# Optimization experiments

Measured on AMD Instinct MI355X. Metric: run time of the kernel, lower is better.

Reference implementation:

```python
import jax, jax.numpy as jnp
import numpy as np

N_NODES = 50000
N_EDGES = 800000
IN_DIM = 64
HID = 128
NUM_GRAPHS = 256


def setup_inputs() -> dict:
    key = jax.random.key(0)
    ks = jax.random.split(key, 20)
    inp = {
        'x': jax.random.normal(ks[0], (N_NODES, IN_DIM), dtype=jnp.float32),
        'edge_index': jax.random.randint(ks[1], (2, N_EDGES), 0, N_NODES, dtype=jnp.int32),
        'batch_idx': jnp.sort(jax.random.randint(ks[2], (N_NODES,), 0, NUM_GRAPHS, dtype=jnp.int32)),
    }
    # GIN layer MLP params (3 layers): Linear(in,hid)->ReLU->Linear(hid,hid)
    dims = [(IN_DIM, HID), (HID, HID), (HID, HID)]
    ki = 3
    for li, (di, dh) in enumerate(dims):
        s1 = 1.0 / np.sqrt(di)
        s2 = 1.0 / np.sqrt(dh)
        inp[f'gin{li}_w1'] = jax.random.uniform(ks[ki], (di, dh), jnp.float32, -s1, s1); ki += 1
        inp[f'gin{li}_b1'] = jnp.zeros((dh,), jnp.float32)
        inp[f'gin{li}_w2'] = jax.random.uniform(ks[ki], (dh, dh), jnp.float32, -s2, s2); ki += 1
        inp[f'gin{li}_b2'] = jnp.zeros((dh,), jnp.float32)
    # head: Linear(2*HID, HID) -> ReLU -> (Dropout eval=id) -> Linear(HID, 1)
    sh = 1.0 / np.sqrt(2 * HID)
    so = 1.0 / np.sqrt(HID)
    inp['head_w1'] = jax.random.uniform(ks[ki], (2 * HID, HID), jnp.float32, -sh, sh); ki += 1
    inp['head_b1'] = jnp.zeros((HID,), jnp.float32)
    inp['head_w2'] = jax.random.uniform(ks[ki], (HID, 1), jnp.float32, -so, so); ki += 1
    inp['head_b2'] = jnp.zeros((1,), jnp.float32)
    return inp


def _gin_layer(h, src, dst, w1, b1, w2, b2):
    # GINConv with eps=0: mlp(x + sum_{j->i} x_j), followed by outer ReLU
    agg = jax.ops.segment_sum(h[src], dst, num_segments=N_NODES)
    z = h + agg
    z = jnp.dot(jax.nn.relu(jnp.dot(z, w1) + b1), w2) + b2
    return jax.nn.relu(z)


def reference(x, edge_index, batch_idx,
              gin0_w1, gin0_b1, gin0_w2, gin0_b2,
              gin1_w1, gin1_b1, gin1_w2, gin1_b2,
              gin2_w1, gin2_b1, gin2_w2, gin2_b2,
              head_w1, head_b1, head_w2, head_b2):
    src, dst = edge_index[0], edge_index[1]
    h = _gin_layer(x, src, dst, gin0_w1, gin0_b1, gin0_w2, gin0_b2)
    h = _gin_layer(h, src, dst, gin1_w1, gin1_b1, gin1_w2, gin1_b2)
    h = _gin_layer(h, src, dst, gin2_w1, gin2_b1, gin2_w2, gin2_b2)
    # meanmax readout over graphs
    cnt = jax.ops.segment_sum(jnp.ones((h.shape[0],), h.dtype), batch_idx,
                              num_segments=NUM_GRAPHS)  # [G]
    ssum = jax.ops.segment_sum(h, batch_idx, num_segments=NUM_GRAPHS)  # [G, HID]
    mean_pool = ssum / jnp.maximum(cnt, 1.0)[:, None]
    max_pool = jax.ops.segment_max(h, batch_idx, num_segments=NUM_GRAPHS)
    max_pool = jnp.where(cnt[:, None] > 0, max_pool, 0.0)
    graph_repr = jnp.concatenate([mean_pool, max_pool], axis=-1)  # [G, 2*HID]
    # fraud head (dropout is identity in eval)
    hh = jax.nn.relu(jnp.dot(graph_repr, head_w1) + head_b1)
    logits = jnp.dot(hh, head_w2) + head_b2  # [G, 1]
    score = jax.nn.sigmoid(logits)
    return score
```

## Files before the change

### kernel.cpp

```cpp
#include <hip/hip_runtime.h>
#include <hip/hip_bf16.h>

#define N_NODES   50000
#define N_EDGES   800000
#define IN_DIM    64
#define HID       128
#define NUM_GRAPHS 256
#define NBUCK     196
#define BCAP      8192
#define CPAD      16

typedef __bf16 bf16x8 __attribute__((ext_vector_type(8)));
typedef unsigned short u16x8 __attribute__((ext_vector_type(8)));
typedef float f32x4 __attribute__((ext_vector_type(4)));

__device__ __forceinline__ float b2f(unsigned short u) {
    return __uint_as_float(((unsigned int)u) << 16);
}
__device__ __forceinline__ unsigned short f2b(float f) {
    unsigned int x = __float_as_uint(f);
    x = (x + 0x7fffu + ((x >> 16) & 1u)) >> 16;
    return (unsigned short)x;
}

__global__ void diag_kernel(unsigned short* out, unsigned short pat) {
    out[threadIdx.x] = pat;
}

__global__ __launch_bounds__(256) void mega_pre_kernel(
    const unsigned short* __restrict__ x,
    const void* w0, const void* w1, const void* w2,
    const void* w3, const void* w4, const void* w5,
    unsigned short* __restrict__ wfbase,
    const int* __restrict__ batch, int* __restrict__ gstart,
    float* __restrict__ psum, unsigned int* __restrict__ pmax,
    const void* hw1, unsigned short* __restrict__ w1t,
    int* __restrict__ bcursor, int* __restrict__ flagp) {
    int b = blockIdx.x;
    int tid = threadIdx.x;

    if (b < 352) {
        __shared__ int cnt;
        if (tid == 0) cnt = 0;
        __syncthreads();
        unsigned short u = x[2 * tid];
        int e = (u >> 7) & 0xff;
        if (e <= 100 || e >= 140) atomicAdd(&cnt, 1);
        __syncthreads();
        int flag = cnt > 64;

        int mat, boff;
        if (b < 32) { mat = 0; boff = b; }
        else { mat = 1 + (b - 32) / 64; boff = (b - 32) % 64; }
        const void* W = mat == 0 ? w0 : mat == 1 ? w1 : mat == 2 ? w2
                      : mat == 3 ? w3 : mat == 4 ? w4 : w5;
        int KC = (mat == 0) ? 2 : 4;
        int idx = boff * 256 + tid;
        int j  = idx & 7;
        int l  = (idx >> 3) & 63;
        int tc = idx >> 9;
        int c  = tc % KC;
        int t  = tc / KC;
        int k  = c * 32 + (l >> 4) * 8 + j;
        int n  = t * 16 + (l & 15);
        unsigned short v = flag ? f2b(((const float*)W)[k * 128 + n])
                                : ((const unsigned short*)W)[k * 128 + n];
        wfbase[mat * 16384 + idx] = v;
    } else if (b < 548) {
        int i = (b - 352) * 256 + tid;
        if (i < NUM_GRAPHS * HID) { psum[i] = 0.0f; pmax[i] = 0u; }
        if (i >= N_NODES) return;
        int b1 = batch[i];
        int b0 = (i == 0) ? -1 : batch[i - 1];
        for (int g = b0 + 1; g <= b1; g++) gstart[g] = i;
        if (i == N_NODES - 1)
            for (int g = b1 + 1; g <= NUM_GRAPHS; g++) gstart[g] = N_NODES;
    } else if (b < 580) {
        __shared__ int cnt;
        if (tid == 0) cnt = 0;
        __syncthreads();
        unsigned short u = x[2 * tid];
        int e = (u >> 7) & 0xff;
        if (e <= 100 || e >= 140) atomicAdd(&cnt, 1);
        __syncthreads();
        int flag = cnt > 64;
        int base = (b - 548) * 1024;
#pragma unroll
        for (int j = 0; j < 4; j++) {
            int idx = base + j * 256 + tid;
            int n = idx >> 8;
            int k = idx & 255;
            unsigned short v = flag ? f2b(((const float*)hw1)[k * 128 + n])
                                    : ((const unsigned short*)hw1)[k * 128 + n];
            w1t[idx] = v;
        }
    } else {
        if (tid < NBUCK) bcursor[tid * CPAD] = tid * BCAP;
        __shared__ int cnt;
        if (tid == 0) cnt = 0;
        __syncthreads();
        int c = 0;
        for (int j = 0; j < 16; j++) {
            unsigned short u = x[2 * (tid * 16 + j)];
            int e = (u >> 7) & 0xff;
            if (e <= 100 || e >= 140) c++;
        }
        atomicAdd(&cnt, c);
        __syncthreads();
        if (tid == 0) *flagp = (cnt > 1024) ? 1 : 0;
    }
}

__global__ __launch_bounds__(1024) void bscatter_kernel(const int* __restrict__ src,
        const int* __restrict__ dst, int* __restrict__ bcursor,
        unsigned int* __restrict__ ebuf) {
    __shared__ int lcnt[NBUCK];
    __shared__ int lbase[NBUCK];
    __shared__ int lcur[NBUCK];
    int tid = threadIdx.x;
    if (tid < NBUCK) lcnt[tid] = 0;
    __syncthreads();
    int e0 = blockIdx.x * 4096;
    int d[4], s[4];
#pragma unroll
    for (int k = 0; k < 4; k++) {
        int e = e0 + k * 1024 + tid;
        if (e < N_EDGES) {
            d[k] = dst[e]; s[k] = src[e];
            atomicAdd(&lcnt[d[k] >> 8], 1);
        } else d[k] = -1;
    }
    __syncthreads();
    if (tid < NBUCK) {
        int c = lcnt[tid];
        lbase[tid] = c ? atomicAdd(&bcursor[tid * CPAD], c) : 0;
        lcur[tid] = 0;
    }
    __syncthreads();
#pragma unroll
    for (int k = 0; k < 4; k++) {
        if (d[k] >= 0) {
            int b = d[k] >> 8;
            int p = lbase[b] + atomicAdd(&lcur[b], 1);
            ebuf[p] = ((unsigned int)(d[k] & 255) << 16) | (unsigned int)s[k];
        }
    }
}

__global__ __launch_bounds__(512) void bsort_kernel(const unsigned int* __restrict__ ebuf,
        const int* __restrict__ bcursor, int* __restrict__ off,
        unsigned short* __restrict__ csr) {
    __shared__ int cntA[256];
    __shared__ int sc[256];
    __shared__ int lcnt[256];
    __shared__ int lcur[256];
    int b = blockIdx.x, tid = threadIdx.x;

    if (tid < 256) {
        int v = (tid < NBUCK) ? (bcursor[tid * CPAD] - tid * BCAP) : 0;
        cntA[tid] = v;
        sc[tid] = v;
    }
    __syncthreads();
    for (int d = 1; d < 256; d <<= 1) {
        int t = (tid >= d && tid < 256) ? sc[tid - d] : 0;
        __syncthreads();
        if (tid < 256) sc[tid] += t;
        __syncthreads();
    }
    int base = sc[b] - cntA[b];
    int cnt  = cntA[b];
    int ebase = b * BCAP;
    __syncthreads();

    if (tid < 256) lcnt[tid] = 0;
    __syncthreads();
    for (int i = tid; i < cnt; i += 512)
        atomicAdd(&lcnt[ebuf[ebase + i] >> 16], 1);
    __syncthreads();
    int v2 = 0;
    if (tid < 256) {
        v2 = lcnt[tid];
        sc[tid] = v2;
    }
    __syncthreads();
    for (int d = 1; d < 256; d <<= 1) {
        int t = (tid >= d && tid < 256) ? sc[tid - d] : 0;
        __syncthreads();
        if (tid < 256) sc[tid] += t;
        __syncthreads();
    }
    if (tid < 256) {
        int excl = sc[tid] - v2;
        lcur[tid] = excl;
        int node = b * 256 + tid;
        if (node < N_NODES) off[node] = base + excl;
    }
    if (b == 0 && tid == 0) off[N_NODES] = N_EDGES;
    __syncthreads();
    for (int i = tid; i < cnt; i += 512) {
        unsigned int ev = ebuf[ebase + i];
        int p = atomicAdd(&lcur[ev >> 16], 1);
        csr[base + p] = (unsigned short)(ev & 0xffffu);
    }
}

template <int K1, bool POOL, bool FROMX>
__global__ __launch_bounds__(256, 3) void fused_gin_kernel(
    const void* __restrict__ X,
    const int* __restrict__ off, const unsigned short* __restrict__ csr,
    const unsigned short* __restrict__ Wf1, const void* __restrict__ bias1,
    const unsigned short* __restrict__ Wf2, const void* __restrict__ bias2,
    unsigned short* __restrict__ Out, int M, const int* __restrict__ flagp,
    const int* __restrict__ batch, float* __restrict__ psum,
    unsigned int* __restrict__ pmax) {
    constexpr int KC1 = K1 / 32;
    __shared__ __align__(16) unsigned short lds_hi[64 * 136];
    __shared__ __align__(16) unsigned short lds_lo[64 * 136];
    __shared__ int batch_lds[64];

    int flag = *flagp;
    int wave = threadIdx.x >> 6;
    int lane = threadIdx.x & 63;
    int m_ = lane & 15;
    int q  = lane >> 4;

    if constexpr (POOL) {
        if (threadIdx.x < 64) {
            int gr = blockIdx.x * 64 + threadIdx.x;
            batch_lds[threadIdx.x] = gr < M ? batch[gr] : -1;
        }
    }

    int np = lane >> 4;
    int l  = lane & 15;
#pragma unroll 1
    for (int p = 0; p < 4; p++) {
        int nl = wave * 16 + p * 4 + np;
        int node = blockIdx.x * 64 + nl;
        int nodec = node < M ? node : (M - 1);
        int s = off[nodec], e = off[nodec + 1];
        if constexpr (FROMX) {
            float a0, a1, a2, a3;
            float b0 = 0.f, b1 = 0.f, b2 = 0.f, b3 = 0.f;
            float c0 = 0.f, c1 = 0.f, c2 = 0.f, c3 = 0.f;
            float d0 = 0.f, d1 = 0.f, d2 = 0.f, d3 = 0.f;
            if (flag) {
                const float4* xp = (const float4*)X;
                float4 u = xp[(size_t)nodec * 16 + l];
                a0 = u.x; a1 = u.y; a2 = u.z; a3 = u.w;
                int i = s;
                for (; i + 7 < e; i += 8) {
                    float4 v0 = xp[(size_t)csr[i] * 16 + l];
                    float4 v1 = xp[(size_t)csr[i + 1] * 16 + l];
                    float4 v2 = xp[(size_t)csr[i + 2] * 16 + l];
                    float4 v3 = xp[(size_t)csr[i + 3] * 16 + l];
                    float4 v4 = xp[(size_t)csr[i + 4] * 16 + l];
                    float4 v5 = xp[(size_t)csr[i + 5] * 16 + l];
                    float4 v6 = xp[(size_t)csr[i + 6] * 16 + l];
                    float4 v7 = xp[(size_t)csr[i + 7] * 16 + l];
                    a0 += v0.x; a1 += v0.y; a2 += v0.z; a3 += v0.w;
                    b0 += v1.x; b1 += v1.y; b2 += v1.z; b3 += v1.w;
                    c0 += v2.x; c1 += v2.y; c2 += v2.z; c3 += v2.w;
                    d0 += v3.x; d1 += v3.y; d2 += v3.z; d3 += v3.w;
                    a0 += v4.x; a1 += v4.y; a2 += v4.z; a3 += v4.w;
                    b0 += v5.x; b1 += v5.y; b2 += v5.z; b3 += v5.w;
                    c0 += v6.x; c1 += v6.y; c2 += v6.z; c3 += v6.w;
                    d0 += v7.x; d1 += v7.y; d2 += v7.z; d3 += v7.w;
                }
                for (; i + 3 < e; i += 4) {
                    float4 v0 = xp[(size_t)csr[i] * 16 + l];
                    float4 v1 = xp[(size_t)csr[i + 1] * 16 + l];
                    float4 v2 = xp[(size_t)csr[i + 2] * 16 + l];
                    float4 v3 = xp[(size_t)csr[i + 3] * 16 + l];
                    a0 += v0.x; a1 += v0.y; a2 += v0.z; a3 += v0.w;
                    b0 += v1.x; b1 += v1.y; b2 += v1.z; b3 += v1.w;
                    c0 += v2.x; c1 += v2.y; c2 += v2.z; c3 += v2.w;
                    d0 += v3.x; d1 += v3.y; d2 += v3.z; d3 += v3.w;
                }
                for (; i < e; i++) {
                    float4 v = xp[(size_t)csr[i] * 16 + l];
                    a0 += v.x; a1 += v.y; a2 += v.z; a3 += v.w;
                }
            } else {
                const ushort4* xp = (const ushort4*)X;
                ushort4 u = xp[(size_t)nodec * 16 + l];
                a0 = b2f(u.x); a1 = b2f(u.y); a2 = b2f(u.z); a3 = b2f(u.w);
                int i = s;
                for (; i + 7 < e; i += 8) {
                    ushort4 v0 = xp[(size_t)csr[i] * 16 + l];
                    ushort4 v1 = xp[(size_t)csr[i + 1] * 16 + l];
                    ushort4 v2 = xp[(size_t)csr[i + 2] * 16 + l];
                    ushort4 v3 = xp[(size_t)csr[i + 3] * 16 + l];
                    ushort4 v4 = xp[(size_t)csr[i + 4] * 16 + l];
                    ushort4 v5 = xp[(size_t)csr[i + 5] * 16 + l];
                    ushort4 v6 = xp[(size_t)csr[i + 6] * 16 + l];
                    ushort4 v7 = xp[(size_t)csr[i + 7] * 16 + l];
                    a0 += b2f(v0.x); a1 += b2f(v0.y); a2 += b2f(v0.z); a3 += b2f(v0.w);
                    b0 += b2f(v1.x); b1 += b2f(v1.y); b2 += b2f(v1.z); b3 += b2f(v1.w);
                    c0 += b2f(v2.x); c1 += b2f(v2.y); c2 += b2f(v2.z); c3 += b2f(v2.w);
                    d0 += b2f(v3.x); d1 += b2f(v3.y); d2 += b2f(v3.z); d3 += b2f(v3.w);
                    a0 += b2f(v4.x); a1 += b2f(v4.y); a2 += b2f(v4.z); a3 += b2f(v4.w);
                    b0 += b2f(v5.x); b1 += b2f(v5.y); b2 += b2f(v5.z); b3 += b2f(v5.w);
                    c0 += b2f(v6.x); c1 += b2f(v6.y); c2 += b2f(v6.z); c3 += b2f(v6.w);
                    d0 += b2f(v7.x); d1 += b2f(v7.y); d2 += b2f(v7.z); d3 += b2f(v7.w);
                }
                for (; i + 3 < e; i += 4) {
                    ushort4 v0 = xp[(size_t)csr[i] * 16 + l];
                    ushort4 v1 = xp[(size_t)csr[i + 1] * 16 + l];
                    ushort4 v2 = xp[(size_t)csr[i + 2] * 16 + l];
                    ushort4 v3 = xp[(size_t)csr[i + 3] * 16 + l];
                    a0 += b2f(v0.x); a1 += b2f(v0.y); a2 += b2f(v0.z); a3 += b2f(v0.w);
                    b0 += b2f(v1.x); b1 += b2f(v1.y); b2 += b2f(v1.z); b3 += b2f(v1.w);
                    c0 += b2f(v2.x); c1 += b2f(v2.y); c2 += b2f(v2.z); c3 += b2f(v2.w);
                    d0 += b2f(v3.x); d1 += b2f(v3.y); d2 += b2f(v3.z); d3 += b2f(v3.w);
                }
                for (; i < e; i++) {
                    ushort4 v = xp[(size_t)csr[i] * 16 + l];
                    a0 += b2f(v.x); a1 += b2f(v.y); a2 += b2f(v.z); a3 += b2f(v.w);
                }
            }
            ushort4 o;
            o.x = f2b(a0 + b0 + c0 + d0);
            o.y = f2b(a1 + b1 + c1 + d1);
            o.z = f2b(a2 + b2 + c2 + d2);
            o.w = f2b(a3 + b3 + c3 + d3);
            *reinterpret_cast<ushort4*>(&lds_hi[nl * 136 + l * 4]) = o;
        } else {
            const u16x8* hp = (const u16x8*)X;
            u16x8 u = hp[(size_t)nodec * 16 + l];
            float a[8], b[8], c[8], d[8];
#pragma unroll
            for (int j = 0; j < 8; j++) { a[j] = b2f(u[j]); b[j] = 0.f; c[j] = 0.f; d[j] = 0.f; }
            int i = s;
            for (; i + 7 < e; i += 8) {
                u16x8 v0 = hp[(size_t)csr[i] * 16 + l];
                u16x8 v1 = hp[(size_t)csr[i + 1] * 16 + l];
                u16x8 v2 = hp[(size_t)csr[i + 2] * 16 + l];
                u16x8 v3 = hp[(size_t)csr[i + 3] * 16 + l];
                u16x8 v4 = hp[(size_t)csr[i + 4] * 16 + l];
                u16x8 v5 = hp[(size_t)csr[i + 5] * 16 + l];
                u16x8 v6 = hp[(size_t)csr[i + 6] * 16 + l];
                u16x8 v7 = hp[(size_t)csr[i + 7] * 16 + l];
#pragma unroll
                for (int j = 0; j < 8; j++) {
                    a[j] += b2f(v0[j]); b[j] += b2f(v1[j]);
                    c[j] += b2f(v2[j]); d[j] += b2f(v3[j]);
                }
#pragma unroll
                for (int j = 0; j < 8; j++) {
                    a[j] += b2f(v4[j]); b[j] += b2f(v5[j]);
                    c[j] += b2f(v6[j]); d[j] += b2f(v7[j]);
                }
            }
            for (; i + 3 < e; i += 4) {
                u16x8 v0 = hp[(size_t)csr[i] * 16 + l];
                u16x8 v1 = hp[(size_t)csr[i + 1] * 16 + l];
                u16x8 v2 = hp[(size_t)csr[i + 2] * 16 + l];
                u16x8 v3 = hp[(size_t)csr[i + 3] * 16 + l];
#pragma unroll
                for (int j = 0; j < 8; j++) {
                    a[j] += b2f(v0[j]); b[j] += b2f(v1[j]);
                    c[j] += b2f(v2[j]); d[j] += b2f(v3[j]);
                }
            }
            for (; i < e; i++) {
                u16x8 v = hp[(size_t)csr[i] * 16 + l];
#pragma unroll
                for (int j = 0; j < 8; j++) a[j] += b2f(v[j]);
            }
            u16x8 o;
#pragma unroll
            for (int j = 0; j < 8; j++) o[j] = f2b(a[j] + b[j] + c[j] + d[j]);
            *reinterpret_cast<u16x8*>(&lds_hi[nl * 136 + l * 8]) = o;
        }
    }

    const unsigned short* wfl1 = Wf1 + lane * 8;
    const unsigned short* wfl2 = Wf2 + lane * 8;
    const unsigned short* zlds = &lds_hi[(wave * 16 + m_) * 136 + q * 8];

    bf16x8 afrag[KC1];
#pragma unroll
    for (int c = 0; c < KC1; c++)
        afrag[c] = *reinterpret_cast<const bf16x8*>(zlds + c * 32);

    float b1v[8], b2v[8];
#pragma unroll
    for (int t = 0; t < 8; t++) {
        int col = t * 16 + m_;
        b1v[t] = flag ? ((const float*)bias1)[col]
                      : b2f(((const unsigned short*)bias1)[col]);
        b2v[t] = flag ? ((const float*)bias2)[col]
                      : b2f(((const unsigned short*)bias2)[col]);
    }

    f32x4 acc[8];
#pragma unroll
    for (int t = 0; t < 8; t++) acc[t] = (f32x4)(0.0f);

    {
        bf16x8 wb[8], wn[8];
#pragma unroll
        for (int t = 0; t < 8; t++)
            wb[t] = *reinterpret_cast<const bf16x8*>(wfl1 + ((t * KC1 + 0) << 9));
#pragma unroll
        for (int c = 0; c < KC1; c++) {
            if (c + 1 < KC1) {
#pragma unroll
                for (int t = 0; t < 8; t++)
                    wn[t] = *reinterpret_cast<const bf16x8*>(wfl1 + ((t * KC1 + c + 1) << 9));
            }
#pragma unroll
            for (int t = 0; t < 8; t++)
                acc[t] = __builtin_amdgcn_mfma_f32_16x16x32_bf16(afrag[c], wb[t], acc[t], 0, 0, 0);
            if (c + 1 < KC1) {
#pragma unroll
                for (int t = 0; t < 8; t++) wb[t] = wn[t];
            }
        }
    }

#pragma unroll
    for (int r = 0; r < 4; r++) {
        int lr = wave * 16 + q * 4 + r;
#pragma unroll
        for (int t = 0; t < 8; t++) {
            int col = t * 16 + m_;
            float v = acc[t][r] + b1v[t];
            v = v > 0.0f ? v : 0.0f;
            unsigned short hb = f2b(v);
            lds_hi[lr * 136 + col] = hb;
            lds_lo[lr * 136 + col] = f2b(v - b2f(hb));
        }
    }

#pragma unroll
    for (int t = 0; t < 8; t++) acc[t] = (f32x4)(0.0f);

    {
        int lr2 = wave * 16 + m_;
        const unsigned short* hibase = &lds_hi[lr2 * 136 + q * 8];
        const unsigned short* lobase = &lds_lo[lr2 * 136 + q * 8];
        bf16x8 wb[8], wn[8];
#pragma unroll
        for (int t = 0; t < 8; t++)
            wb[t] = *reinterpret_cast<const bf16x8*>(wfl2 + ((t * 4 + 0) << 9));
#pragma unroll
        for (int c = 0; c < 4; c++) {
            if (c < 3) {
#pragma unroll
                for (int t = 0; t < 8; t++)
                    wn[t] = *reinterpret_cast<const bf16x8*>(wfl2 + ((t * 4 + c + 1) << 9));
            }
            bf16x8 ahi = *reinterpret_cast<const bf16x8*>(hibase + c * 32);
            bf16x8 alo = *reinterpret_cast<const bf16x8*>(lobase + c * 32);
#pragma unroll
            for (int t = 0; t < 8; t++) {
                acc[t] = __builtin_amdgcn_mfma_f32_16x16x32_bf16(ahi, wb[t], acc[t], 0, 0, 0);
                acc[t] = __builtin_amdgcn_mfma_f32_16x16x32_bf16(alo, wb[t], acc[t], 0, 0, 0);
            }
            if (c < 3) {
#pragma unroll
                for (int t = 0; t < 8; t++) wb[t] = wn[t];
            }
        }
    }

#pragma unroll
    for (int r = 0; r < 4; r++) {
        int lr = wave * 16 + q * 4 + r;
        int orow = blockIdx.x * 64 + lr;
#pragma unroll
        for (int t = 0; t < 8; t++) {
            int col = t * 16 + m_;
            float v = acc[t][r] + b2v[t];
            v = v > 0.0f ? v : 0.0f;
            if constexpr (POOL) {
                lds_hi[lr * 136 + col] = f2b(v);
            } else {
                if (orow < M) Out[(size_t)orow * HID + col] = f2b(v);
            }
        }
    }

    if constexpr (POOL) {
        __syncthreads();
        int f = threadIdx.x;
        if (f < HID) {
            int cur = -1;
            float sum = 0.0f, mx = 0.0f;
            for (int rrow = 0; rrow < 64; rrow++) {
                int g = batch_lds[rrow];
                if (g < 0) break;
                float v = b2f(lds_hi[rrow * 136 + f]);
                if (g == cur) {
                    sum += v;
                    mx = fmaxf(mx, v);
                } else {
                    if (cur >= 0) {
                        atomicAdd(&psum[cur * HID + f], sum);
                        atomicMax(&pmax[cur * HID + f], __float_as_uint(mx));
                    }
                    cur = g; sum = v; mx = v;
                }
            }
            if (cur >= 0) {
                atomicAdd(&psum[cur * HID + f], sum);
                atomicMax(&pmax[cur * HID + f], __float_as_uint(mx));
            }
        }
    }
}

__global__ __launch_bounds__(128) void head_kernel(
    const float* __restrict__ psum, const unsigned int* __restrict__ pmax,
    const int* __restrict__ gstart,
    const unsigned short* __restrict__ w1t,
    const void* __restrict__ b1, const void* __restrict__ w2,
    const void* __restrict__ b2,
    void* __restrict__ out, const int* __restrict__ flagp) {
    int g = blockIdx.x;
    int n = threadIdx.x;
    int flag = *flagp;
    __shared__ float repr[2 * HID];
    __shared__ float red[HID];

    float c = (float)(gstart[g + 1] - gstart[g]);
    float inv = 1.0f / fmaxf(c, 1.0f);
    repr[n]       = psum[g * HID + n] * inv;
    repr[HID + n] = __uint_as_float(pmax[g * HID + n]);
    __syncthreads();

    const u16x8* wp = (const u16x8*)(w1t + n * 256);
    float a0 = 0.f, a1 = 0.f, a2 = 0.f, a3 = 0.f;
#pragma unroll
    for (int c8 = 0; c8 < 32; c8 += 4) {
        u16x8 w0 = wp[c8 + 0];
        u16x8 w1 = wp[c8 + 1];
        u16x8 w2v = wp[c8 + 2];
        u16x8 w3 = wp[c8 + 3];
#pragma unroll
        for (int j = 0; j < 8; j++) {
            a0 += repr[(c8 + 0) * 8 + j] * b2f(w0[j]);
            a1 += repr[(c8 + 1) * 8 + j] * b2f(w1[j]);
            a2 += repr[(c8 + 2) * 8 + j] * b2f(w2v[j]);
            a3 += repr[(c8 + 3) * 8 + j] * b2f(w3[j]);
        }
    }
    float b1v = flag ? ((const float*)b1)[n] : b2f(((const unsigned short*)b1)[n]);
    float acc = a0 + a1 + a2 + a3 + b1v;
    acc = fmaxf(acc, 0.0f);

    float w2s = flag ? ((const float*)w2)[n] : b2f(((const unsigned short*)w2)[n]);
    red[n] = acc * w2s;
    __syncthreads();
    for (int s = 64; s > 0; s >>= 1) {
        if (n < s) red[n] += red[n + s];
        __syncthreads();
    }
    if (n == 0) {
        float b2v = flag ? ((const float*)b2)[0] : b2f(((const unsigned short*)b2)[0]);
        float logit = red[0] + b2v;
        float sv = 1.0f / (1.0f + expf(-logit));
        if (flag) ((float*)out)[g] = sv;
        else      ((unsigned short*)out)[g] = f2b(sv);
    }
}

extern "C" void kernel_launch(void* const* d_in, const int* in_sizes, int n_in,
                              void* d_out, int out_size, void* d_ws, size_t ws_size,
                              hipStream_t stream) {
    const int* edge = (const int*)d_in[1];
    const int* srcv = edge;
    const int* dstv = edge + N_EDGES;
    const int* batch = (const int*)d_in[2];

    char* ws = (char*)d_ws;
    unsigned short* A = (unsigned short*)ws;
    unsigned short* B = (unsigned short*)(ws + 12800000);
    unsigned int* ebuf = (unsigned int*)(ws + 25600000);
    unsigned short* csr = (unsigned short*)(ws + 32100000);
    int* off    = (int*)(ws + 33700000);
    unsigned short* wfbase = (unsigned short*)(ws + 33904000);
    float* psum  = (float*)(ws + 34100608);
    unsigned int* pmax = (unsigned int*)(ws + 34231680);
    int* gstart  = (int*)(ws + 34363776);
    int* flagp   = (int*)(ws + 34365824);
    unsigned short* w1t = (unsigned short*)(ws + 34366848);
    int* bcursor = (int*)(ws + 34432384);

    const size_t NEED = 34500000;
    if (ws_size < NEED) {
        unsigned int k = 0;
        while ((((size_t)1) << (k + 1)) <= ws_size && k < 62) k++;
        diag_kernel<<<1, 256, 0, stream>>>((unsigned short*)d_out,
                                           (unsigned short)(0x4000 | (k & 63)));
        return;
    }

    mega_pre_kernel<<<581, 256, 0, stream>>>(
        (const unsigned short*)d_in[0],
        d_in[3], d_in[5], d_in[7], d_in[9], d_in[11], d_in[13], wfbase,
        batch, gstart, psum, pmax, d_in[15], w1t, bcursor, flagp);

    const int EB = (N_EDGES + 4095) / 4096;
    bscatter_kernel<<<EB, 1024, 0, stream>>>(srcv, dstv, bcursor, ebuf);
    bsort_kernel<<<NBUCK, 512, 0, stream>>>(ebuf, bcursor, off, csr);

    const int GEMM_GRID = (N_NODES + 63) / 64;

    fused_gin_kernel<64, false, true><<<GEMM_GRID, 256, 0, stream>>>(
        d_in[0], off, csr,
        wfbase + 0 * 16384, d_in[4], wfbase + 1 * 16384, d_in[6],
        A, N_NODES, flagp, batch, psum, pmax);

    fused_gin_kernel<128, false, false><<<GEMM_GRID, 256, 0, stream>>>(
        A, off, csr,
        wfbase + 2 * 16384, d_in[8], wfbase + 3 * 16384, d_in[10],
        B, N_NODES, flagp, batch, psum, pmax);

    fused_gin_kernel<128, true, false><<<GEMM_GRID, 256, 0, stream>>>(
        B, off, csr,
        wfbase + 4 * 16384, d_in[12], wfbase + 5 * 16384, d_in[14],
        A , N_NODES, flagp, batch, psum, pmax);

    head_kernel<<<NUM_GRAPHS, 128, 0, stream>>>(psum, pmax, gstart, w1t,
                                                d_in[16], d_in[17], d_in[18],
                                                d_out, flagp);
}
```

Before: 248.6 us.

## Sub-sort CSR neighbors by source-node quarter to improve gather locality

The bucket sort kernel now keys edges by destination node together with a 2-bit coarse source range, so each node's neighbor list is grouped by source quarter. The intent is better cache locality in the later gather of neighbor features across the three GIN layers. The block size grows to 1024 threads with a 1024-entry scan, which adds scan steps and LDS atomics in the sort.

New measurement: 247.3 us. No clear change (-0.5%).

```diff
diff --git a/kernel.cpp b/kernel.cpp
--- a/kernel.cpp
+++ b/kernel.cpp
@@ -147,61 +147,65 @@
     }
 }
 
-__global__ __launch_bounds__(512) void bsort_kernel(const unsigned int* __restrict__ ebuf,
+__global__ __launch_bounds__(1024) void bsort_kernel(const unsigned int* __restrict__ ebuf,
         const int* __restrict__ bcursor, int* __restrict__ off,
         unsigned short* __restrict__ csr) {
     __shared__ int cntA[256];
-    __shared__ int sc[256];
-    __shared__ int lcnt[256];
-    __shared__ int lcur[256];
+    __shared__ int scB[256];
+    __shared__ int sc[1024];
+    __shared__ int lcur[1024];
     int b = blockIdx.x, tid = threadIdx.x;
 
     if (tid < 256) {
         int v = (tid < NBUCK) ? (bcursor[tid * CPAD] - tid * BCAP) : 0;
         cntA[tid] = v;
-        sc[tid] = v;
+        scB[tid] = v;
     }
     __syncthreads();
     for (int d = 1; d < 256; d <<= 1) {
-        int t = (tid >= d && tid < 256) ? sc[tid - d] : 0;
-        __syncthreads();
-        if (tid < 256) sc[tid] += t;
-        __syncthreads();
-    }
-    int base = sc[b] - cntA[b];
+        int t = (tid >= d && tid < 256) ? scB[tid - d] : 0;
+        __syncthreads();
+        if (tid < 256) scB[tid] += t;
+        __syncthreads();
+    }
+    int base = scB[b] - cntA[b];
     int cnt  = cntA[b];
     int ebase = b * BCAP;
     __syncthreads();
 
-    if (tid < 256) lcnt[tid] = 0;
-    __syncthreads();
-    for (int i = tid; i < cnt; i += 512)
-        atomicAdd(&lcnt[ebuf[ebase + i] >> 16], 1);
-    __syncthreads();
-    int v2 = 0;
-    if (tid < 256) {
-        v2 = lcnt[tid];
-        sc[tid] = v2;
-    }
-    __syncthreads();
-    for (int d = 1; d < 256; d <<= 1) {
-        int t = (tid >= d && tid < 256) ? sc[tid - d] : 0;
-        __syncthreads();
-        if (tid < 256) sc[tid] += t;
-        __syncthreads();
-    }
-    if (tid < 256) {
-        int excl = sc[tid] - v2;
-        lcur[tid] = excl;
-        int node = b * 256 + tid;
+    sc[tid] = 0;
+    __syncthreads();
+    for (int i = tid; i < cnt; i += 1024) {
+        unsigned int ev = ebuf[ebase + i];
+        int s = (int)(ev & 0xffffu);
+        int key = (int)((ev >> 16) << 2) |
+                  ((s >= 12500) + (s >= 25000) + (s >= 37500));
+        atomicAdd(&sc[key], 1);
+    }
+    __syncthreads();
+    int v2 = sc[tid];
+    __syncthreads();
+    for (int d = 1; d < 1024; d <<= 1) {
+        int t = (tid >= d) ? sc[tid - d] : 0;
+        __syncthreads();
+        sc[tid] += t;
+        __syncthreads();
+    }
+    int excl = sc[tid] - v2;
+    lcur[tid] = excl;
+    if ((tid & 3) == 0) {
+        int node = b * 256 + (tid >> 2);
         if (node < N_NODES) off[node] = base + excl;
     }
     if (b == 0 && tid == 0) off[N_NODES] = N_EDGES;
     __syncthreads();
-    for (int i = tid; i < cnt; i += 512) {
+    for (int i = tid; i < cnt; i += 1024) {
         unsigned int ev = ebuf[ebase + i];
-        int p = atomicAdd(&lcur[ev >> 16], 1);
-        csr[base + p] = (unsigned short)(ev & 0xffffu);
+        int s = (int)(ev & 0xffffu);
+        int key = (int)((ev >> 16) << 2) |
+                  ((s >= 12500) + (s >= 25000) + (s >= 37500));
+        int p = atomicAdd(&lcur[key], 1);
+        csr[base + p] = (unsigned short)s;
     }
 }
 
@@ -606,7 +610,7 @@
 
     const int EB = (N_EDGES + 4095) / 4096;
     bscatter_kernel<<<EB, 1024, 0, stream>>>(srcv, dstv, bcursor, ebuf);
-    bsort_kernel<<<NBUCK, 512, 0, stream>>>(ebuf, bcursor, off, csr);
+    bsort_kernel<<<NBUCK, 1024, 0, stream>>>(ebuf, bcursor, off, csr);
 
     const int GEMM_GRID = (N_NODES + 63) / 64;
 
```
